# Performance work log

Hardware: AMD Instinct MI355X
Metric: run time of the kernel (lower is better)

Reference implementation:

```python
import jax, jax.numpy as jnp
import numpy as np

B, S, HID, H = 2, 2048, 2048, 16
D = HID // H  # 128 head dim
SCALE = 1.0 / np.sqrt(D)


def setup_inputs() -> dict:
    key = jax.random.key(0)
    ks = jax.random.split(key, 10)
    w = lambda k, shp: (jax.random.normal(k, shp, jnp.float32) * 0.02)
    x = jax.random.normal(ks[0], (B, S, HID), jnp.float32)
    mask = jnp.tril(jnp.ones((S, S), jnp.bool_))[None, None]  # causal [1,1,S,S]
    return {
        "x": x,
        "mask": mask,
        "Wq": w(ks[1], (HID, HID)), "bq": w(ks[2], (HID,)),
        "Wk": w(ks[3], (D, HID)),   "bk": w(ks[4], (D,)),
        "Wv": w(ks[5], (D, HID)),   "bv": w(ks[6], (D,)),
        "Wo": w(ks[7], (HID, HID)), "bo": w(ks[8], (HID,)),
    }


def reference(x, mask, Wq, bq, Wk, bk, Wv, bv, Wo, bo):
    b, s, _ = x.shape
    # projections (torch Linear: x @ W.T + b)
    q = (x @ Wq.T + bq).reshape(b, s, H, D).transpose(0, 2, 1, 3)  # [B,H,S,D]
    k = x @ Wk.T + bk  # [B,S,D] single KV head
    v = x @ Wv.T + bv  # [B,S,D]
    scores = jnp.einsum("bhqd,bkd->bhqk", q, k) * SCALE  # [B,H,S,S]
    scores = jnp.where(mask, scores, -jnp.inf)
    attn = jax.nn.softmax(scores, axis=-1)
    out = jnp.einsum("bhqk,bkd->bhqd", attn, v)  # [B,H,S,D]
    out = out.transpose(0, 2, 1, 3).reshape(b, s, HID)
    return out @ Wo.T + bo
```

## Files before the change

kernel.cpp:

```cpp
#include <hip/hip_runtime.h>


#define S_LEN 2048
#define HID_  2048
#define D_    128
#define NQKV  2304

typedef __attribute__((ext_vector_type(8))) short bf16x8;
typedef __attribute__((ext_vector_type(4))) float f32x4;
typedef __attribute__((ext_vector_type(16))) float f32x16;

__device__ __forceinline__ unsigned short f2b(float f) {
  union { float f; unsigned int u; } a; a.f = f;
  unsigned int u = a.u;
  return (unsigned short)((u + 0x7fffu + ((u >> 16) & 1u)) >> 16);
}

__device__ __forceinline__ float b2f(unsigned short s) {
  union { unsigned int u; float f; } a; a.u = ((unsigned int)s) << 16;
  return a.f;
}

__device__ __forceinline__ void load_lds16(const void* g, void* l) {
  __builtin_amdgcn_global_load_lds(
      (const __attribute__((address_space(1))) void*)g,
      (__attribute__((address_space(3))) void*)l, 16, 0, 0);
}

__device__ __forceinline__ f32x4 mfma16(bf16x8 a, bf16x8 b, f32x4 c) {
  return __builtin_amdgcn_mfma_f32_16x16x32_bf16(a, b, c, 0, 0, 0);
}

__device__ __forceinline__ f32x16 mfma32(bf16x8 a, bf16x8 b, f32x16 c) {
  return __builtin_amdgcn_mfma_f32_32x32x16_bf16(a, b, c, 0, 0, 0);
}

__device__ __forceinline__ unsigned int cvtpk(float lo, float hi) {
  unsigned int r;
  asm volatile("v_cvt_pk_bf16_f32 %0, %1, %2" : "=v"(r) : "v"(lo), "v"(hi));
  return r;
}


__global__ void cast_f32_bf16_k(const float* __restrict__ in,
                                unsigned short* __restrict__ out, int n4) {
  const int idx = blockIdx.x * 256 + threadIdx.x;
  if (idx < n4) {
    const float4 v = ((const float4*)in)[idx];
    ushort4 o;
    o.x = f2b(v.x); o.y = f2b(v.y); o.z = f2b(v.z); o.w = f2b(v.w);
    ((ushort4*)out)[idx] = o;
  }
}

__global__ void build_wcat_k(const float* __restrict__ Wq,
                             const float* __restrict__ Wk,
                             const float* __restrict__ Wv,
                             const float* __restrict__ bq,
                             const float* __restrict__ bk,
                             const float* __restrict__ bv,
                             unsigned short* __restrict__ Wcat,
                             float* __restrict__ bcat,
                             float* __restrict__ Kmax) {
  const int idx = blockIdx.x * 256 + threadIdx.x;
  const int i = idx * 4;
  const int row = i >> 11;
  const int col = i & 2047;
  const float* src;
  if (row < 2048)      src = Wq + (size_t)row * 2048 + col;
  else if (row < 2176) src = Wk + (size_t)(row - 2048) * 2048 + col;
  else                 src = Wv + (size_t)(row - 2176) * 2048 + col;
  const float4 v = *(const float4*)src;
  ushort4 o;
  o.x = f2b(v.x); o.y = f2b(v.y); o.z = f2b(v.z); o.w = f2b(v.w);
  *(ushort4*)(Wcat + i) = o;
  if (idx < NQKV)
    bcat[idx] = (idx < 2048) ? bq[idx] : (idx < 2176) ? bk[idx - 2048] : bv[idx - 2176];
  if (idx < 2) Kmax[idx] = 0.f;
}

__global__ __launch_bounds__(256)
void transpose_v(const unsigned short* __restrict__ QKV,
                 unsigned short* __restrict__ Vt) {
  __shared__ unsigned short tile[64][136];
  const int tid = threadIdx.x;
  const int s0  = blockIdx.x * 64;
  const int b   = blockIdx.y;
  const int row = tid >> 2;
  const int cb  = (tid & 3) * 32;
  const unsigned short* src = QKV + (size_t)(b * S_LEN + s0 + row) * NQKV + 2176 + cb;
#pragma unroll
  for (int i = 0; i < 4; ++i)
    *(bf16x8*)&tile[row][cb + i * 8] = *(const bf16x8*)(src + i * 8);
  __syncthreads();
  const int d  = tid >> 1;
  const int sc = (tid & 1) * 32;
  unsigned short* dst = Vt + ((size_t)b * D_ + d) * S_LEN + s0 + sc;
#pragma unroll
  for (int i = 0; i < 4; ++i) {
    bf16x8 vv;
#pragma unroll
    for (int e = 0; e < 8; ++e) vv[e] = tile[sc + i * 8 + e][d];
    *(bf16x8*)(dst + i * 8) = vv;
  }
}

__global__ __launch_bounds__(256)
void kmax_k(const unsigned short* __restrict__ QKV, float* __restrict__ Kmax) {
  __shared__ float red[256];
  const int tid = threadIdx.x;
  const int b = blockIdx.x >> 3;
  const int s = (blockIdx.x & 7) * 256 + tid;
  const unsigned short* kp = QKV + (size_t)(b * S_LEN + s) * NQKV + 2048;
  float sum = 0.f;
#pragma unroll
  for (int i = 0; i < 16; ++i) {
    bf16x8 v = *(const bf16x8*)(kp + i * 8);
#pragma unroll
    for (int e = 0; e < 8; ++e) { const float f = b2f((unsigned short)v[e]); sum += f * f; }
  }
  red[tid] = sum;
  __syncthreads();
  for (int off = 128; off > 0; off >>= 1) {
    if (tid < off) red[tid] = fmaxf(red[tid], red[tid + off]);
    __syncthreads();
  }
  if (tid == 0) atomicMax((unsigned int*)(Kmax + b), __float_as_uint(red[0]));
}


template <int OUT_F32, int NJ>
__global__ __launch_bounds__(512, 2)
void gemm_nt2(const unsigned short* __restrict__ A,
              const unsigned short* __restrict__ Bm,
              const float* __restrict__ bias,
              void* __restrict__ Cv,
              int N, int K) {
  constexpr int BN = 64 * NJ;
  __shared__ __align__(16) char As[3][128 * 128];
  __shared__ __align__(16) char Bs[3][BN * 128];

  const int tid  = threadIdx.x;
  const int lane = tid & 63;
  const int wv   = tid >> 6;
  const int wr   = wv >> 2;
  const int wc   = wv & 3;
  const int g    = lane >> 4, r = lane & 15;

  const int nwg  = gridDim.x;
  const int bid  = blockIdx.x;
  const int sbid = (bid & 7) * (nwg >> 3) + (bid >> 3);
  const int nx   = N / BN;
  const int m0   = (sbid / nx) * 128;
  const int n0   = (sbid % nx) * BN;
  const int NT   = K >> 6;

  const size_t Kb = (size_t)K * 2;
  const char* Ab = (const char*)A + (size_t)m0 * Kb;
  const char* Bb = (const char*)Bm + (size_t)n0 * Kb;

#define STAGE_A(bufi, t)                                                       \
  {                                                                            \
    const int kb_ = (t) * 128;                                                 \
    _Pragma("unroll")                                                          \
    for (int i_ = 0; i_ < 2; ++i_) {                                           \
      const int ch_ = tid + 512 * i_;                                          \
      const int rr_ = ch_ >> 3;                                                \
      const int sl_ = (ch_ & 7) ^ (rr_ & 7);                                   \
      load_lds16(Ab + (size_t)rr_ * Kb + kb_ + sl_ * 16, As[bufi] + ch_ * 16); \
    }                                                                          \
  }
#define STAGE_B(bufi, t)                                                       \
  {                                                                            \
    const int kb_ = (t) * 128;                                                 \
    _Pragma("unroll")                                                          \
    for (int i_ = 0; i_ < NJ; ++i_) {                                          \
      const int ch_ = tid + 512 * i_;                                          \
      const int rr_ = ch_ >> 3;                                                \
      const int sl_ = (ch_ & 7) ^ (rr_ & 7);                                   \
      load_lds16(Bb + (size_t)rr_ * Kb + kb_ + sl_ * 16, Bs[bufi] + ch_ * 16); \
    }                                                                          \
  }

  f32x4 acc[4][NJ] = {};
  const int s0 = ((g ^ (r & 7)) << 4);
  const int s1 = (((4 | g) ^ (r & 7)) << 4);

  STAGE_A(0, 0) STAGE_B(0, 0) STAGE_A(1, 1) STAGE_B(1, 1)

  asm volatile("s_waitcnt vmcnt(%0)" :: "i"(NJ + 2) : "memory");
  __builtin_amdgcn_s_barrier();
  __builtin_amdgcn_sched_barrier(0);

  for (int t = 0; t < NT; ++t) {
    const char* as = As[t % 3];
    const char* bs = Bs[t % 3];
    const int nb = (t + 2) % 3;
    const bool pf = (t + 2 < NT);

    bf16x8 af[4], bfr[NJ];
#pragma unroll
    for (int i = 0; i < 4; ++i)
      af[i] = *(const bf16x8*)(as + ((wr * 64 + i * 16 + r) << 7) + s0);
#pragma unroll
    for (int j = 0; j < NJ; ++j)
      bfr[j] = *(const bf16x8*)(bs + ((wc * 16 * NJ + j * 16 + r) << 7) + s0);
    if (pf) STAGE_A(nb, t + 2)
    __builtin_amdgcn_s_barrier();
    __builtin_amdgcn_sched_barrier(0);
    asm volatile("s_waitcnt lgkmcnt(0)" ::: "memory");
    __builtin_amdgcn_sched_barrier(0);
    __builtin_amdgcn_s_setprio(1);
#pragma unroll
    for (int i = 0; i < 4; ++i)
#pragma unroll
      for (int j = 0; j < NJ; ++j)
        acc[i][j] = mfma16(af[i], bfr[j], acc[i][j]);
    __builtin_amdgcn_s_setprio(0);
    __builtin_amdgcn_sched_barrier(0);

#pragma unroll
    for (int i = 0; i < 4; ++i)
      af[i] = *(const bf16x8*)(as + ((wr * 64 + i * 16 + r) << 7) + s1);
#pragma unroll
    for (int j = 0; j < NJ; ++j)
      bfr[j] = *(const bf16x8*)(bs + ((wc * 16 * NJ + j * 16 + r) << 7) + s1);
    if (pf) STAGE_B(nb, t + 2)
    __builtin_amdgcn_s_barrier();
    __builtin_amdgcn_sched_barrier(0);
    asm volatile("s_waitcnt lgkmcnt(0)" ::: "memory");
    __builtin_amdgcn_sched_barrier(0);
    __builtin_amdgcn_s_setprio(1);
#pragma unroll
    for (int i = 0; i < 4; ++i)
#pragma unroll
      for (int j = 0; j < NJ; ++j)
        acc[i][j] = mfma16(af[i], bfr[j], acc[i][j]);
    __builtin_amdgcn_s_setprio(0);

    if (pf) { asm volatile("s_waitcnt vmcnt(%0)" :: "i"(NJ + 2) : "memory"); }
    else    { asm volatile("s_waitcnt vmcnt(0)" ::: "memory"); }
    __builtin_amdgcn_s_barrier();
    __builtin_amdgcn_sched_barrier(0);
  }

#pragma unroll
  for (int i = 0; i < 4; ++i) {
    const int row = m0 + wr * 64 + i * 16 + g * 4;
#pragma unroll
    for (int j = 0; j < NJ; ++j) {
      const int col = n0 + wc * 16 * NJ + j * 16 + r;
      const float bb = bias[col];
#pragma unroll
      for (int e = 0; e < 4; ++e) {
        const float v = acc[i][j][e] + bb;
        if (OUT_F32) ((float*)Cv)[(size_t)(row + e) * N + col] = v;
        else ((unsigned short*)Cv)[(size_t)(row + e) * N + col] = f2b(v);
      }
    }
  }
#undef STAGE_A
#undef STAGE_B
}


__global__ __launch_bounds__(256, 2)
void mqa_attn(const unsigned short* __restrict__ QKV,
              const unsigned short* __restrict__ Vt,
              const float* __restrict__ Kmax,
              unsigned short* __restrict__ Ob,
              unsigned short* __restrict__ Pacc,
              float* __restrict__ Pl) {
  __shared__ __align__(16) char Ks[2][64 * 256];
  __shared__ __align__(16) char Vs[2][64 * 256];

  const int tid  = threadIdx.x;
  const int lane = tid & 63;
  const int wv   = tid >> 6;
  const int ln   = lane & 31;
  const int hi   = lane >> 5;
  const int x    = blockIdx.x;
  const int bhq  = x & 7;
  const int b    = bhq >> 2;
  const int hq   = bhq & 3;
  const int widx = x >> 3;
  int qt, t0, te, chunk;
  if (widx < 32)      { qt = 32 + widx; t0 = 0;  te = 16;         chunk = 0; }
  else if (widx < 64) { qt = 95 - widx; t0 = 16; te = qt / 2 + 1; chunk = 1; }
  else                { qt = 95 - widx; t0 = 0;  te = qt / 2 + 1; chunk = -1; }
  const int h    = hq * 4 + wv;
  const int qw   = qt * 32;
  const int lastT = qt / 2;

  bf16x8 qf[8];
  {
    const unsigned short* qp =
        QKV + (size_t)(b * S_LEN + qw + ln) * NQKV + h * D_ + hi * 8;
#pragma unroll
    for (int ch = 0; ch < 8; ++ch) qf[ch] = *(const bf16x8*)(qp + ch * 16);
  }

  const float sscale = 0.08838834764831845f * 1.4426950408889634f;
  float qn2 = 0.f;
#pragma unroll
  for (int ch = 0; ch < 8; ++ch)
#pragma unroll
    for (int e = 0; e < 8; ++e) {
      const float qv = b2f((unsigned short)qf[ch][e]);
      qn2 += qv * qv;
    }
  qn2 += __shfl_xor(qn2, 32);
  const float m0c = sqrtf(qn2) * sqrtf(Kmax[b]) * sscale + 1.0f;

  const char* kbc = (const char*)(QKV + (size_t)(b * S_LEN) * NQKV + 2048);
  const char* vbc = (const char*)(Vt + (size_t)b * D_ * S_LEN);

  f32x16 acc[4] = {};
  float accl = 0.f;

#define STAGE(bufi, t)                                                         \
  {                                                                            \
    const int kv0_ = (t) * 64;                                                 \
    _Pragma("unroll")                                                          \
    for (int i_ = 0; i_ < 4; ++i_) {                                           \
      const int ch_ = tid + 256 * i_;                                          \
      const int kr_ = ch_ >> 4;                                                \
      const int kg_ = (ch_ & 15) ^ (kr_ & 15);                                 \
      load_lds16(kbc + (size_t)(kv0_ + kr_) * (NQKV * 2) + kg_ * 16,           \
                 Ks[bufi] + ch_ * 16);                                         \
      const int vg_ = (ch_ & 15) ^ (kr_ & 15);                                 \
      const int vd_ = kr_ * 2 + (vg_ >> 3);                                    \
      load_lds16(vbc + (size_t)vd_ * (S_LEN * 2) + kv0_ * 2 + (vg_ & 7) * 16,  \
                 Vs[bufi] + ch_ * 16);                                         \
    }                                                                          \
  }

  STAGE(0, t0);
  int cur = 0;

  for (int t = t0; t < te; ++t) {
    __syncthreads();
    if (t + 1 < te) STAGE(cur ^ 1, t + 1);

    const char* ksb = Ks[cur];
    const char* vsb = Vs[cur];
    const int kv0 = t * 64;
    const bool last = (t == lastT);
    const bool doUp = (kv0 + 32 <= qw + 31);
    cur ^= 1;

    f32x16 sA = {}, sB = {};
    __builtin_amdgcn_s_setprio(1);
#pragma unroll
    for (int ch = 0; ch < 8; ++ch) {
      const int slot0 = (2 * ch + hi) ^ (ln & 15);
      const bf16x8 kf0 = *(const bf16x8*)(ksb + ln * 256 + slot0 * 16);
      sA = mfma32(kf0, qf[ch], sA);
      if (doUp) {
        const bf16x8 kf1 = *(const bf16x8*)(ksb + (32 + ln) * 256 + slot0 * 16);
        sB = mfma32(kf1, qf[ch], sB);
      }
    }
    __builtin_amdgcn_s_setprio(0);

    bf16x8 pa0, pa1, pa2, pa3;
    float p[16];

#define SOFTMAX(sv, kvtbase)                                                   \
    _Pragma("unroll")                                                          \
    for (int rr = 0; rr < 16; ++rr) {                                          \
      float e = sv[rr] * sscale - m0c;                                         \
      if (last) {                                                              \
        const int kva = (kvtbase) + (rr & 3) + 8 * (rr >> 2) + 4 * hi;         \
        e = (kva <= qw + ln) ? e : -__builtin_inff();                          \
      }                                                                        \
      const float pv_ = __builtin_amdgcn_exp2f(e);                             \
      p[rr] = pv_; accl += pv_;                                                \
    }

#define PACK2(fa, fb)                                                          \
    {                                                                          \
      const unsigned int A0 = cvtpk(p[0], p[1]),   A1 = cvtpk(p[2], p[3]);     \
      const unsigned int B0 = cvtpk(p[4], p[5]),   B1 = cvtpk(p[6], p[7]);     \
      const unsigned int C0 = cvtpk(p[8], p[9]),   C1 = cvtpk(p[10], p[11]);   \
      const unsigned int D0 = cvtpk(p[12], p[13]), D1 = cvtpk(p[14], p[15]);   \
      unsigned int X0 = hi ? A0 : B0, X1 = hi ? A1 : B1;                       \
      unsigned int Y0 = hi ? C0 : D0, Y1 = hi ? C1 : D1;                       \
      X0 = (unsigned int)__shfl_xor((int)X0, 32);                              \
      X1 = (unsigned int)__shfl_xor((int)X1, 32);                              \
      Y0 = (unsigned int)__shfl_xor((int)Y0, 32);                              \
      Y1 = (unsigned int)__shfl_xor((int)Y1, 32);                              \
      union { unsigned int w[4]; bf16x8 v; } ua, ub;                           \
      ua.w[0] = hi ? X0 : A0; ua.w[1] = hi ? X1 : A1;                          \
      ua.w[2] = hi ? B0 : X0; ua.w[3] = hi ? B1 : X1;                          \
      ub.w[0] = hi ? Y0 : C0; ub.w[1] = hi ? Y1 : C1;                          \
      ub.w[2] = hi ? D0 : Y0; ub.w[3] = hi ? D1 : Y1;                          \
      fa = ua.v; fb = ub.v;                                                    \
    }

    SOFTMAX(sA, kv0)
    PACK2(pa0, pa1)
    if (doUp) {
      SOFTMAX(sB, kv0 + 32)
      PACK2(pa2, pa3)
    }

    __builtin_amdgcn_s_setprio(1);
#pragma unroll
    for (int dt = 0; dt < 4; ++dt) {
      const int vrow = dt * 16 + (ln >> 1);
      const int gb   = (ln & 1) << 3;
      {
        const int sl = (gb + 0 + hi) ^ (vrow & 15);
        const bf16x8 vf = *(const bf16x8*)(vsb + vrow * 256 + sl * 16);
        acc[dt] = mfma32(pa0, vf, acc[dt]);
      }
      {
        const int sl = (gb + 2 + hi) ^ (vrow & 15);
        const bf16x8 vf = *(const bf16x8*)(vsb + vrow * 256 + sl * 16);
        acc[dt] = mfma32(pa1, vf, acc[dt]);
      }
      if (doUp) {
        {
          const int sl = (gb + 4 + hi) ^ (vrow & 15);
          const bf16x8 vf = *(const bf16x8*)(vsb + vrow * 256 + sl * 16);
          acc[dt] = mfma32(pa2, vf, acc[dt]);
        }
        {
          const int sl = (gb + 6 + hi) ^ (vrow & 15);
          const bf16x8 vf = *(const bf16x8*)(vsb + vrow * 256 + sl * 16);
          acc[dt] = mfma32(pa3, vf, acc[dt]);
        }
      }
    }
    __builtin_amdgcn_s_setprio(0);
#undef SOFTMAX
#undef PACK2
  }

  const float lf = accl + __shfl_xor(accl, 32);

  if (chunk < 0) {
    const float linv = 1.0f / lf;
    unsigned short* ob = Ob + (size_t)(b * S_LEN + qw) * HID_ + h * D_ + ln;
#pragma unroll
    for (int rr = 0; rr < 16; ++rr) {
      const int qr = (rr & 3) + 8 * (rr >> 2) + 4 * hi;
      const float li = __shfl(linv, qr);
#pragma unroll
      for (int dt = 0; dt < 4; ++dt)
        ob[(size_t)qr * HID_ + dt * 32] = f2b(acc[dt][rr] * li);
    }
  } else {
    const int slot = ((chunk * 2 + b) * 16 + h) * 32 + (qt - 32);
    unsigned short* pa = Pacc + (size_t)slot * 32 * 128 + ln;
#pragma unroll
    for (int rr = 0; rr < 16; ++rr) {
      const int qr = (rr & 3) + 8 * (rr >> 2) + 4 * hi;
#pragma unroll
      for (int dt = 0; dt < 4; ++dt)
        pa[qr * 128 + dt * 32] = f2b(acc[dt][rr]);
    }
    if (hi == 0) Pl[slot * 32 + ln] = lf;
  }
#undef STAGE
}

__global__ __launch_bounds__(256)
void combine_k(const unsigned short* __restrict__ Pacc,
               const float* __restrict__ Pl,
               unsigned short* __restrict__ Ob) {
  const int x  = blockIdx.x;
  const int qs = x & 31;
  const int h  = (x >> 5) & 15;
  const int b  = x >> 9;
  const int tid = threadIdx.x;
  const int q  = tid >> 3;
  const int dp = (tid & 7) * 16;
  const int s0 = (b * 16 + h) * 32 + qs;
  const int s1 = ((2 + b) * 16 + h) * 32 + qs;
  const float inv = 1.0f / (Pl[s0 * 32 + q] + Pl[s1 * 32 + q]);
  const unsigned short* a0 = Pacc + ((size_t)s0 * 32 + q) * 128 + dp;
  const unsigned short* a1 = Pacc + ((size_t)s1 * 32 + q) * 128 + dp;
  unsigned short* ob =
      Ob + (size_t)(b * S_LEN + (32 + qs) * 32 + q) * HID_ + h * D_ + dp;
  const bf16x8 v0a = *(const bf16x8*)a0, v0b = *(const bf16x8*)(a0 + 8);
  const bf16x8 v1a = *(const bf16x8*)a1, v1b = *(const bf16x8*)(a1 + 8);
  bf16x8 oa, obv;
#pragma unroll
  for (int e = 0; e < 8; ++e) {
    oa[e]  = (short)f2b((b2f((unsigned short)v0a[e]) + b2f((unsigned short)v1a[e])) * inv);
    obv[e] = (short)f2b((b2f((unsigned short)v0b[e]) + b2f((unsigned short)v1b[e])) * inv);
  }
  *(bf16x8*)ob = oa;
  *(bf16x8*)(ob + 8) = obv;
}


extern "C" void kernel_launch(void* const* d_in, const int* in_sizes, int n_in,
                              void* d_out, int out_size, void* d_ws, size_t ws_size,
                              hipStream_t stream) {
  (void)in_sizes; (void)n_in; (void)out_size; (void)ws_size;
  const float* x  = (const float*)d_in[0];
  const float* Wq = (const float*)d_in[2];
  const float* bq = (const float*)d_in[3];
  const float* Wk = (const float*)d_in[4];
  const float* bk = (const float*)d_in[5];
  const float* Wv = (const float*)d_in[6];
  const float* bv = (const float*)d_in[7];
  const float* Wo = (const float*)d_in[8];
  const float* bo = (const float*)d_in[9];
  float* out = (float*)d_out;

  char* p = (char*)d_ws;
  unsigned short* xb   = (unsigned short*)p;  p += (size_t)4096 * 2048 * 2;
  unsigned short* Wcat = (unsigned short*)p;  p += (size_t)2304 * 2048 * 2;
  float*          bcat = (float*)p;           p += 16384;
  unsigned short* Wob  = (unsigned short*)p;  p += (size_t)2048 * 2048 * 2;
  unsigned short* QKV  = (unsigned short*)p;  p += (size_t)4096 * 2304 * 2;
  unsigned short* Vt   = (unsigned short*)p;  p += (size_t)2 * 128 * 2048 * 2;
  float*          Kmax = (float*)p;           p += 64;
  unsigned short* Pacc = (unsigned short*)p;  p += (size_t)2048 * 32 * 128 * 2;
  float*          Pl   = (float*)p;           p += (size_t)2048 * 32 * 4;
  unsigned short* Ob   = xb;

  cast_f32_bf16_k<<<8192, 256, 0, stream>>>(x, xb, 2097152);
  build_wcat_k<<<4608, 256, 0, stream>>>(Wq, Wk, Wv, bq, bk, bv, Wcat, bcat, Kmax);
  cast_f32_bf16_k<<<4096, 256, 0, stream>>>(Wo, Wob, 1048576);
  gemm_nt2<0, 3><<<384, 512, 0, stream>>>(xb, Wcat, bcat, QKV, 2304, 2048);
  transpose_v<<<dim3(32, 2), 256, 0, stream>>>(QKV, Vt);
  kmax_k<<<16, 256, 0, stream>>>(QKV, Kmax);
  mqa_attn<<<768, 256, 0, stream>>>(QKV, Vt, Kmax, Ob, Pacc, Pl);
  combine_k<<<1024, 256, 0, stream>>>(Pacc, Pl, Ob);
  gemm_nt2<1, 4><<<256, 512, 0, stream>>>(Ob, Wob, bo, out, 2048, 2048);
}
```

Measured before the change: 191.2 us.

## Switch GEMMs to 32x32 MFMA with 128x256 tiles and fewer barriers

Both projection GEMMs move from 16x16x32 MFMA tiles to 32x32x16 MFMA with each wave computing a 64x64 output block, and the block tile widens to 128x256. The QKV GEMM's grid drops from 384 to 288 blocks. The k-loop interleaves LDS fragment loads with MFMAs and keeps a single barrier per iteration instead of three, which is meant to cut LDS traffic per flop and synchronisation overhead. In exchange, 288 blocks may fill the CUs unevenly, the larger B buffer raises LDS usage, and the per-iteration ordering of LDS reads against prefetch stores is looser.

```diff
diff --git a/kernel.cpp b/kernel.cpp
--- a/kernel.cpp
+++ b/kernel.cpp
@@ -25,10 +25,6 @@
   __builtin_amdgcn_global_load_lds(
       (const __attribute__((address_space(1))) void*)g,
       (__attribute__((address_space(3))) void*)l, 16, 0, 0);
-}
-
-__device__ __forceinline__ f32x4 mfma16(bf16x8 a, bf16x8 b, f32x4 c) {
-  return __builtin_amdgcn_mfma_f32_16x16x32_bf16(a, b, c, 0, 0, 0);
 }
 
 __device__ __forceinline__ f32x16 mfma32(bf16x8 a, bf16x8 b, f32x16 c) {
@@ -129,37 +125,37 @@
 }
 
 
-template <int OUT_F32, int NJ>
+template <int OUT_F32>
 __global__ __launch_bounds__(512, 2)
-void gemm_nt2(const unsigned short* __restrict__ A,
-              const unsigned short* __restrict__ Bm,
-              const float* __restrict__ bias,
-              void* __restrict__ Cv,
-              int N, int K) {
-  constexpr int BN = 64 * NJ;
+void gemm3(const unsigned short* __restrict__ A,
+           const unsigned short* __restrict__ Bm,
+           const float* __restrict__ bias,
+           void* __restrict__ Cv,
+           int N, int K) {
   __shared__ __align__(16) char As[3][128 * 128];
-  __shared__ __align__(16) char Bs[3][BN * 128];
+  __shared__ __align__(16) char Bs[3][256 * 128];
 
   const int tid  = threadIdx.x;
   const int lane = tid & 63;
   const int wv   = tid >> 6;
   const int wr   = wv >> 2;
   const int wc   = wv & 3;
-  const int g    = lane >> 4, r = lane & 15;
+  const int ln   = lane & 31;
+  const int hi   = lane >> 5;
 
   const int nwg  = gridDim.x;
   const int bid  = blockIdx.x;
   const int sbid = (bid & 7) * (nwg >> 3) + (bid >> 3);
-  const int nx   = N / BN;
+  const int nx   = N >> 8;
   const int m0   = (sbid / nx) * 128;
-  const int n0   = (sbid % nx) * BN;
+  const int n0   = (sbid % nx) * 256;
   const int NT   = K >> 6;
 
   const size_t Kb = (size_t)K * 2;
   const char* Ab = (const char*)A + (size_t)m0 * Kb;
   const char* Bb = (const char*)Bm + (size_t)n0 * Kb;
 
-#define STAGE_A(bufi, t)                                                       \
+#define STG_A(bufi, t)                                                         \
   {                                                                            \
     const int kb_ = (t) * 128;                                                 \
     _Pragma("unroll")                                                          \
@@ -170,11 +166,11 @@
       load_lds16(Ab + (size_t)rr_ * Kb + kb_ + sl_ * 16, As[bufi] + ch_ * 16); \
     }                                                                          \
   }
-#define STAGE_B(bufi, t)                                                       \
+#define STG_B(bufi, t)                                                         \
   {                                                                            \
     const int kb_ = (t) * 128;                                                 \
     _Pragma("unroll")                                                          \
-    for (int i_ = 0; i_ < NJ; ++i_) {                                          \
+    for (int i_ = 0; i_ < 4; ++i_) {                                           \
       const int ch_ = tid + 512 * i_;                                          \
       const int rr_ = ch_ >> 3;                                                \
       const int sl_ = (ch_ & 7) ^ (rr_ & 7);                                   \
@@ -182,85 +178,89 @@
     }                                                                          \
   }
 
-  f32x4 acc[4][NJ] = {};
-  const int s0 = ((g ^ (r & 7)) << 4);
-  const int s1 = (((4 | g) ^ (r & 7)) << 4);
-
-  STAGE_A(0, 0) STAGE_B(0, 0) STAGE_A(1, 1) STAGE_B(1, 1)
-
-  asm volatile("s_waitcnt vmcnt(%0)" :: "i"(NJ + 2) : "memory");
+  f32x16 acc00 = {}, acc01 = {}, acc10 = {}, acc11 = {};
+
+  const int xr   = ln & 7;
+  const int aro0 = (wr * 64 + ln) * 128;
+  const int aro1 = aro0 + 32 * 128;
+  const int bro0 = (wc * 64 + ln) * 128;
+  const int bro1 = bro0 + 32 * 128;
+  const int ss0 = (((0 + hi) ^ xr) << 4);
+  const int ss1 = (((2 + hi) ^ xr) << 4);
+  const int ss2 = (((4 + hi) ^ xr) << 4);
+  const int ss3 = (((6 + hi) ^ xr) << 4);
+
+  STG_A(0, 0) STG_B(0, 0) STG_A(1, 1) STG_B(1, 1)
+  asm volatile("s_waitcnt vmcnt(6)" ::: "memory");
   __builtin_amdgcn_s_barrier();
   __builtin_amdgcn_sched_barrier(0);
 
   for (int t = 0; t < NT; ++t) {
-    const char* as = As[t % 3];
-    const char* bs = Bs[t % 3];
+    const char* as = (const char*)As[t % 3];
+    const char* bs = (const char*)Bs[t % 3];
     const int nb = (t + 2) % 3;
     const bool pf = (t + 2 < NT);
 
-    bf16x8 af[4], bfr[NJ];
-#pragma unroll
-    for (int i = 0; i < 4; ++i)
-      af[i] = *(const bf16x8*)(as + ((wr * 64 + i * 16 + r) << 7) + s0);
-#pragma unroll
-    for (int j = 0; j < NJ; ++j)
-      bfr[j] = *(const bf16x8*)(bs + ((wc * 16 * NJ + j * 16 + r) << 7) + s0);
-    if (pf) STAGE_A(nb, t + 2)
-    __builtin_amdgcn_s_barrier();
-    __builtin_amdgcn_sched_barrier(0);
-    asm volatile("s_waitcnt lgkmcnt(0)" ::: "memory");
-    __builtin_amdgcn_sched_barrier(0);
+    bf16x8 xa0 = *(const bf16x8*)(as + aro0 + ss0);
+    bf16x8 xa1 = *(const bf16x8*)(as + aro1 + ss0);
+    bf16x8 xb0 = *(const bf16x8*)(bs + bro0 + ss0);
+    bf16x8 xb1 = *(const bf16x8*)(bs + bro1 + ss0);
+    if (pf) STG_A(nb, t + 2)
+    bf16x8 ya0 = *(const bf16x8*)(as + aro0 + ss1);
+    bf16x8 ya1 = *(const bf16x8*)(as + aro1 + ss1);
+    bf16x8 yb0 = *(const bf16x8*)(bs + bro0 + ss1);
+    bf16x8 yb1 = *(const bf16x8*)(bs + bro1 + ss1);
     __builtin_amdgcn_s_setprio(1);
-#pragma unroll
-    for (int i = 0; i < 4; ++i)
-#pragma unroll
-      for (int j = 0; j < NJ; ++j)
-        acc[i][j] = mfma16(af[i], bfr[j], acc[i][j]);
+    acc00 = mfma32(xa0, xb0, acc00); acc01 = mfma32(xa0, xb1, acc01);
+    acc10 = mfma32(xa1, xb0, acc10); acc11 = mfma32(xa1, xb1, acc11);
     __builtin_amdgcn_s_setprio(0);
-    __builtin_amdgcn_sched_barrier(0);
-
-#pragma unroll
-    for (int i = 0; i < 4; ++i)
-      af[i] = *(const bf16x8*)(as + ((wr * 64 + i * 16 + r) << 7) + s1);
-#pragma unroll
-    for (int j = 0; j < NJ; ++j)
-      bfr[j] = *(const bf16x8*)(bs + ((wc * 16 * NJ + j * 16 + r) << 7) + s1);
-    if (pf) STAGE_B(nb, t + 2)
-    __builtin_amdgcn_s_barrier();
-    __builtin_amdgcn_sched_barrier(0);
-    asm volatile("s_waitcnt lgkmcnt(0)" ::: "memory");
-    __builtin_amdgcn_sched_barrier(0);
+    if (pf) STG_B(nb, t + 2)
+    xa0 = *(const bf16x8*)(as + aro0 + ss2);
+    xa1 = *(const bf16x8*)(as + aro1 + ss2);
+    xb0 = *(const bf16x8*)(bs + bro0 + ss2);
+    xb1 = *(const bf16x8*)(bs + bro1 + ss2);
     __builtin_amdgcn_s_setprio(1);
-#pragma unroll
-    for (int i = 0; i < 4; ++i)
-#pragma unroll
-      for (int j = 0; j < NJ; ++j)
-        acc[i][j] = mfma16(af[i], bfr[j], acc[i][j]);
+    acc00 = mfma32(ya0, yb0, acc00); acc01 = mfma32(ya0, yb1, acc01);
+    acc10 = mfma32(ya1, yb0, acc10); acc11 = mfma32(ya1, yb1, acc11);
     __builtin_amdgcn_s_setprio(0);
-
-    if (pf) { asm volatile("s_waitcnt vmcnt(%0)" :: "i"(NJ + 2) : "memory"); }
-    else    { asm volatile("s_waitcnt vmcnt(0)" ::: "memory"); }
-    __builtin_amdgcn_s_barrier();
-    __builtin_amdgcn_sched_barrier(0);
-  }
-
-#pragma unroll
-  for (int i = 0; i < 4; ++i) {
-    const int row = m0 + wr * 64 + i * 16 + g * 4;
-#pragma unroll
-    for (int j = 0; j < NJ; ++j) {
-      const int col = n0 + wc * 16 * NJ + j * 16 + r;
-      const float bb = bias[col];
-#pragma unroll
-      for (int e = 0; e < 4; ++e) {
-        const float v = acc[i][j][e] + bb;
-        if (OUT_F32) ((float*)Cv)[(size_t)(row + e) * N + col] = v;
-        else ((unsigned short*)Cv)[(size_t)(row + e) * N + col] = f2b(v);
-      }
-    }
-  }
-#undef STAGE_A
-#undef STAGE_B
+    ya0 = *(const bf16x8*)(as + aro0 + ss3);
+    ya1 = *(const bf16x8*)(as + aro1 + ss3);
+    yb0 = *(const bf16x8*)(bs + bro0 + ss3);
+    yb1 = *(const bf16x8*)(bs + bro1 + ss3);
+    __builtin_amdgcn_s_setprio(1);
+    acc00 = mfma32(xa0, xb0, acc00); acc01 = mfma32(xa0, xb1, acc01);
+    acc10 = mfma32(xa1, xb0, acc10); acc11 = mfma32(xa1, xb1, acc11);
+    acc00 = mfma32(ya0, yb0, acc00); acc01 = mfma32(ya0, yb1, acc01);
+    acc10 = mfma32(ya1, yb0, acc10); acc11 = mfma32(ya1, yb1, acc11);
+    __builtin_amdgcn_s_setprio(0);
+
+    if (t + 1 < NT) {
+      if (pf) { asm volatile("s_waitcnt vmcnt(6)" ::: "memory"); }
+      else    { asm volatile("s_waitcnt vmcnt(0)" ::: "memory"); }
+      __builtin_amdgcn_s_barrier();
+      __builtin_amdgcn_sched_barrier(0);
+    }
+  }
+
+#define EPI(accv, fm, fn)                                                      \
+  {                                                                            \
+    const int col = n0 + wc * 64 + (fn) * 32 + ln;                             \
+    const float bb = bias[col];                                                \
+    const int rb = m0 + wr * 64 + (fm) * 32 + 4 * hi;                          \
+    _Pragma("unroll")                                                          \
+    for (int rg = 0; rg < 4; ++rg)                                             \
+      _Pragma("unroll")                                                        \
+      for (int e = 0; e < 4; ++e) {                                            \
+        const float v = accv[rg * 4 + e] + bb;                                 \
+        const int row = rb + rg * 8 + e;                                       \
+        if (OUT_F32) ((float*)Cv)[(size_t)row * N + col] = v;                  \
+        else ((unsigned short*)Cv)[(size_t)row * N + col] = f2b(v);            \
+      }                                                                        \
+  }
+  EPI(acc00, 0, 0) EPI(acc01, 0, 1) EPI(acc10, 1, 0) EPI(acc11, 1, 1)
+#undef EPI
+#undef STG_A
+#undef STG_B
 }
 
 
@@ -527,10 +527,10 @@
   cast_f32_bf16_k<<<8192, 256, 0, stream>>>(x, xb, 2097152);
   build_wcat_k<<<4608, 256, 0, stream>>>(Wq, Wk, Wv, bq, bk, bv, Wcat, bcat, Kmax);
   cast_f32_bf16_k<<<4096, 256, 0, stream>>>(Wo, Wob, 1048576);
-  gemm_nt2<0, 3><<<384, 512, 0, stream>>>(xb, Wcat, bcat, QKV, 2304, 2048);
+  gemm3<0><<<288, 512, 0, stream>>>(xb, Wcat, bcat, QKV, 2304, 2048);
   transpose_v<<<dim3(32, 2), 256, 0, stream>>>(QKV, Vt);
   kmax_k<<<16, 256, 0, stream>>>(QKV, Kmax);
   mqa_attn<<<768, 256, 0, stream>>>(QKV, Vt, Kmax, Ob, Pacc, Pl);
   combine_k<<<1024, 256, 0, stream>>>(Pacc, Pl, Ob);
-  gemm_nt2<1, 4><<<256, 512, 0, stream>>>(Ob, Wob, bo, out, 2048, 2048);
-}
+  gemm3<1><<<256, 512, 0, stream>>>(Ob, Wob, bo, out, 2048, 2048);
+}
```

Result: slower. 242.6 us (+26.9%).

## Replace GEMM with 128x128 tile, 256-thread, K=32 triple-buffered kernel

Applied to the files above, without the earlier changes.

Replaces the 512-thread GEMM, which used 128xBN tiles with K=64 steps and two barriers per step, with a 256-thread kernel on 128x128 tiles, K=32 steps and a single barrier per iteration. It also allows three blocks per CU. The smaller per-block LDS footprint and larger grid (576 and 512 blocks) aim to raise occupancy and cut barrier overhead. The cost is less data reuse per K step, twice as many loop iterations, and a K=32 swizzle pattern that may produce more LDS bank conflicts.

```diff
diff --git a/kernel.cpp b/kernel.cpp
--- a/kernel.cpp
+++ b/kernel.cpp
@@ -129,127 +129,93 @@
 }
 
 
-template <int OUT_F32, int NJ>
-__global__ __launch_bounds__(512, 2)
-void gemm_nt2(const unsigned short* __restrict__ A,
-              const unsigned short* __restrict__ Bm,
-              const float* __restrict__ bias,
-              void* __restrict__ Cv,
-              int N, int K) {
-  constexpr int BN = 64 * NJ;
-  __shared__ __align__(16) char As[3][128 * 128];
-  __shared__ __align__(16) char Bs[3][BN * 128];
+template <int OUT_F32>
+__global__ __launch_bounds__(256, 3)
+void gemm4(const unsigned short* __restrict__ A,
+           const unsigned short* __restrict__ Bm,
+           const float* __restrict__ bias,
+           void* __restrict__ Cv,
+           int N, int K) {
+  __shared__ __align__(16) char As[3][128 * 64];
+  __shared__ __align__(16) char Bs[3][128 * 64];
 
   const int tid  = threadIdx.x;
   const int lane = tid & 63;
   const int wv   = tid >> 6;
-  const int wr   = wv >> 2;
-  const int wc   = wv & 3;
+  const int wr   = wv >> 1, wc = wv & 1;
   const int g    = lane >> 4, r = lane & 15;
 
   const int nwg  = gridDim.x;
   const int bid  = blockIdx.x;
   const int sbid = (bid & 7) * (nwg >> 3) + (bid >> 3);
-  const int nx   = N / BN;
+  const int nx   = N >> 7;
   const int m0   = (sbid / nx) * 128;
-  const int n0   = (sbid % nx) * BN;
-  const int NT   = K >> 6;
+  const int n0   = (sbid % nx) * 128;
+  const int NT   = K >> 5;
 
   const size_t Kb = (size_t)K * 2;
   const char* Ab = (const char*)A + (size_t)m0 * Kb;
   const char* Bb = (const char*)Bm + (size_t)n0 * Kb;
 
-#define STAGE_A(bufi, t)                                                       \
+#define STG(bufi, t)                                                           \
   {                                                                            \
-    const int kb_ = (t) * 128;                                                 \
+    const int kb_ = (t) * 64;                                                  \
     _Pragma("unroll")                                                          \
     for (int i_ = 0; i_ < 2; ++i_) {                                           \
-      const int ch_ = tid + 512 * i_;                                          \
-      const int rr_ = ch_ >> 3;                                                \
-      const int sl_ = (ch_ & 7) ^ (rr_ & 7);                                   \
+      const int ch_ = tid + 256 * i_;                                          \
+      const int rr_ = ch_ >> 2;                                                \
+      const int sl_ = (ch_ & 3) ^ (rr_ & 3);                                   \
       load_lds16(Ab + (size_t)rr_ * Kb + kb_ + sl_ * 16, As[bufi] + ch_ * 16); \
-    }                                                                          \
-  }
-#define STAGE_B(bufi, t)                                                       \
-  {                                                                            \
-    const int kb_ = (t) * 128;                                                 \
-    _Pragma("unroll")                                                          \
-    for (int i_ = 0; i_ < NJ; ++i_) {                                          \
-      const int ch_ = tid + 512 * i_;                                          \
-      const int rr_ = ch_ >> 3;                                                \
-      const int sl_ = (ch_ & 7) ^ (rr_ & 7);                                   \
       load_lds16(Bb + (size_t)rr_ * Kb + kb_ + sl_ * 16, Bs[bufi] + ch_ * 16); \
     }                                                                          \
   }
 
-  f32x4 acc[4][NJ] = {};
-  const int s0 = ((g ^ (r & 7)) << 4);
-  const int s1 = (((4 | g) ^ (r & 7)) << 4);
-
-  STAGE_A(0, 0) STAGE_B(0, 0) STAGE_A(1, 1) STAGE_B(1, 1)
-
-  asm volatile("s_waitcnt vmcnt(%0)" :: "i"(NJ + 2) : "memory");
+  f32x4 acc[4][4] = {};
+  const int ss = ((g ^ (r & 3)) << 4);
+
+  STG(0, 0) STG(1, 1)
+  asm volatile("s_waitcnt vmcnt(4)" ::: "memory");
   __builtin_amdgcn_s_barrier();
   __builtin_amdgcn_sched_barrier(0);
 
   for (int t = 0; t < NT; ++t) {
-    const char* as = As[t % 3];
-    const char* bs = Bs[t % 3];
-    const int nb = (t + 2) % 3;
+    const char* as = (const char*)As[t % 3];
+    const char* bs = (const char*)Bs[t % 3];
     const bool pf = (t + 2 < NT);
 
-    bf16x8 af[4], bfr[NJ];
+    bf16x8 af[4], bfr[4];
 #pragma unroll
     for (int i = 0; i < 4; ++i)
-      af[i] = *(const bf16x8*)(as + ((wr * 64 + i * 16 + r) << 7) + s0);
-#pragma unroll
-    for (int j = 0; j < NJ; ++j)
-      bfr[j] = *(const bf16x8*)(bs + ((wc * 16 * NJ + j * 16 + r) << 7) + s0);
-    if (pf) STAGE_A(nb, t + 2)
-    __builtin_amdgcn_s_barrier();
-    __builtin_amdgcn_sched_barrier(0);
+      af[i] = *(const bf16x8*)(as + (wr * 64 + i * 16 + r) * 64 + ss);
+#pragma unroll
+    for (int j = 0; j < 4; ++j)
+      bfr[j] = *(const bf16x8*)(bs + (wc * 64 + j * 16 + r) * 64 + ss);
+    if (pf) STG((t + 2) % 3, t + 2)
+
     asm volatile("s_waitcnt lgkmcnt(0)" ::: "memory");
     __builtin_amdgcn_sched_barrier(0);
     __builtin_amdgcn_s_setprio(1);
 #pragma unroll
     for (int i = 0; i < 4; ++i)
 #pragma unroll
-      for (int j = 0; j < NJ; ++j)
+      for (int j = 0; j < 4; ++j)
         acc[i][j] = mfma16(af[i], bfr[j], acc[i][j]);
     __builtin_amdgcn_s_setprio(0);
-    __builtin_amdgcn_sched_barrier(0);
-
-#pragma unroll
-    for (int i = 0; i < 4; ++i)
-      af[i] = *(const bf16x8*)(as + ((wr * 64 + i * 16 + r) << 7) + s1);
-#pragma unroll
-    for (int j = 0; j < NJ; ++j)
-      bfr[j] = *(const bf16x8*)(bs + ((wc * 16 * NJ + j * 16 + r) << 7) + s1);
-    if (pf) STAGE_B(nb, t + 2)
-    __builtin_amdgcn_s_barrier();
-    __builtin_amdgcn_sched_barrier(0);
-    asm volatile("s_waitcnt lgkmcnt(0)" ::: "memory");
-    __builtin_amdgcn_sched_barrier(0);
-    __builtin_amdgcn_s_setprio(1);
-#pragma unroll
-    for (int i = 0; i < 4; ++i)
-#pragma unroll
-      for (int j = 0; j < NJ; ++j)
-        acc[i][j] = mfma16(af[i], bfr[j], acc[i][j]);
-    __builtin_amdgcn_s_setprio(0);
-
-    if (pf) { asm volatile("s_waitcnt vmcnt(%0)" :: "i"(NJ + 2) : "memory"); }
-    else    { asm volatile("s_waitcnt vmcnt(0)" ::: "memory"); }
-    __builtin_amdgcn_s_barrier();
-    __builtin_amdgcn_sched_barrier(0);
+
+    if (t + 1 < NT) {
+      if (pf) { asm volatile("s_waitcnt vmcnt(4)" ::: "memory"); }
+      else    { asm volatile("s_waitcnt vmcnt(0)" ::: "memory"); }
+      __builtin_amdgcn_s_barrier();
+      __builtin_amdgcn_sched_barrier(0);
+    }
   }
 
 #pragma unroll
   for (int i = 0; i < 4; ++i) {
     const int row = m0 + wr * 64 + i * 16 + g * 4;
 #pragma unroll
-    for (int j = 0; j < NJ; ++j) {
-      const int col = n0 + wc * 16 * NJ + j * 16 + r;
+    for (int j = 0; j < 4; ++j) {
+      const int col = n0 + wc * 64 + j * 16 + r;
       const float bb = bias[col];
 #pragma unroll
       for (int e = 0; e < 4; ++e) {
@@ -259,8 +225,7 @@
       }
     }
   }
-#undef STAGE_A
-#undef STAGE_B
+#undef STG
 }
 
 
@@ -527,10 +492,10 @@
   cast_f32_bf16_k<<<8192, 256, 0, stream>>>(x, xb, 2097152);
   build_wcat_k<<<4608, 256, 0, stream>>>(Wq, Wk, Wv, bq, bk, bv, Wcat, bcat, Kmax);
   cast_f32_bf16_k<<<4096, 256, 0, stream>>>(Wo, Wob, 1048576);
-  gemm_nt2<0, 3><<<384, 512, 0, stream>>>(xb, Wcat, bcat, QKV, 2304, 2048);
+  gemm4<0><<<576, 256, 0, stream>>>(xb, Wcat, bcat, QKV, 2304, 2048);
   transpose_v<<<dim3(32, 2), 256, 0, stream>>>(QKV, Vt);
   kmax_k<<<16, 256, 0, stream>>>(QKV, Kmax);
   mqa_attn<<<768, 256, 0, stream>>>(QKV, Vt, Kmax, Ob, Pacc, Pl);
   combine_k<<<1024, 256, 0, stream>>>(Pacc, Pl, Ob);
-  gemm_nt2<1, 4><<<256, 512, 0, stream>>>(Ob, Wob, bo, out, 2048, 2048);
-}
+  gemm4<1><<<512, 256, 0, stream>>>(Ob, Wob, bo, out, 2048, 2048);
+}
```

Result: faster. 181.9 us (-4.9%).
